# Performance work log

Measured on AMD Instinct MI355X. Metric: run time of the kernel, lower is better.

## Reference

```python
import jax, jax.numpy as jnp
import numpy as np

N_ATOMS = 50000
N_EDGES = 1_600_000
H = 128
EPS = 1e-3  # keras BatchNormalization default epsilon


def _bn(x, gamma, beta, mean, var):
    # inference-mode batch norm with moving statistics
    return gamma * (x - mean) * jax.lax.rsqrt(var + EPS) + beta


def setup_inputs() -> dict:
    key = jax.random.key(0)
    ks = jax.random.split(key, 16)
    s = 0.05
    D1 = H + 1
    inp = {
        "atom_embedding": jax.random.normal(ks[0], (N_ATOMS, H), jnp.float32),
        "bond_embedding": jax.random.normal(ks[1], (N_EDGES, H), jnp.float32),
        "indices_i": jax.random.randint(ks[2], (N_EDGES,), 0, N_ATOMS, dtype=jnp.int32),
        "indices_j": jax.random.randint(ks[3], (N_EDGES,), 0, N_ATOMS, dtype=jnp.int32),
        # preprocess: Dense(3H -> H+1, no bias) + BN, Dense(H+1 -> H+1, no bias) + BN
        "W1": jax.random.normal(ks[4], (3 * H, D1), jnp.float32) * s,
        "g1": jnp.ones((D1,), jnp.float32),
        "b1": jnp.zeros((D1,), jnp.float32),
        "m1": jnp.zeros((D1,), jnp.float32),
        "v1": jnp.ones((D1,), jnp.float32),
        "W2": jax.random.normal(ks[5], (D1, D1), jnp.float32) * s,
        "g2": jnp.ones((D1,), jnp.float32),
        "b2": jnp.zeros((D1,), jnp.float32),
        "m2": jnp.zeros((D1,), jnp.float32),
        "v2": jnp.ones((D1,), jnp.float32),
        # two residual layers, each: x + (x@w1+b1)@w2+b2 (activation=None)
        "r1w1": jax.random.normal(ks[6], (H, H), jnp.float32) * s,
        "r1b1": jnp.zeros((H,), jnp.float32),
        "r1w2": jax.random.normal(ks[7], (H, H), jnp.float32) * s,
        "r1b2": jnp.zeros((H,), jnp.float32),
        "r2w1": jax.random.normal(ks[8], (H, H), jnp.float32) * s,
        "r2b1": jnp.zeros((H,), jnp.float32),
        "r2w2": jax.random.normal(ks[9], (H, H), jnp.float32) * s,
        "r2b2": jnp.zeros((H,), jnp.float32),
    }
    return inp


def reference(atom_embedding, bond_embedding, indices_i, indices_j,
              W1, g1, b1, m1, v1, W2, g2, b2, m2, v2,
              r1w1, r1b1, r1w2, r1b2, r2w1, r2b1, r2w2, r2b2):
    # gather endpoints: [E, H]
    ai = atom_embedding[indices_i]
    aj = atom_embedding[indices_j]
    x = jnp.concatenate([ai, bond_embedding, aj], axis=-1)  # [E, 3H]
    x = _bn(x @ W1, g1, b1, m1, v1)  # [E, H+1]
    x = _bn(x @ W2, g2, b2, m2, v2)  # [E, H+1]
    msg = x[:, :1] * x[:, 1:]  # gate * message -> [E, H]
    atom = atom_embedding + jax.ops.segment_sum(msg, indices_i, num_segments=N_ATOMS)
    # residual MLPs (activation=None -> identity)
    atom = atom + (atom @ r1w1 + r1b1) @ r1w2 + r1b2
    atom = atom + (atom @ r2w1 + r2b1) @ r2w2 + r2b2
    return atom
```

## Files before the change

### kernel.cpp

```cpp
#include <hip/hip_runtime.h>

#define NA 50000
#define NE 1600000
#define HH 128
#define D1 129
#define EPS 1e-3f

typedef __bf16 bf16_t;
typedef bf16_t bf16x8 __attribute__((ext_vector_type(8)));
typedef bf16_t bf16x4 __attribute__((ext_vector_type(4)));
typedef float f32x4 __attribute__((ext_vector_type(4)));

#define OFF_A1   0
#define OFF_C1   129
#define OFF_A2   258
#define OFF_C2   387
#define OFF_WEFF 516
#define OFF_DVEC (OFF_WEFF + 384*129)
#define OFF_Q1   (OFF_DVEC + 129)
#define OFF_Q2   (OFF_Q1 + 128*128)
#define OFF_q1   (OFF_Q2 + 128*128)
#define OFF_q2   (OFF_q1 + 128)
#define OFF_QF   (OFF_q2 + 128)
#define OFF_qf   (OFF_QF + 128*128)
#define OFF_WMT  (((OFF_qf + 128) + 3) & ~3)
#define OFF_WTT  (OFF_WMT + 9216)
#define OFF_WBT  (OFF_WTT + 9216)
#define OFF_QFT  (OFF_WBT + 9216)
#define OFF_PI   (OFF_QFT + 8192)
#define OFF_PJ   (OFF_PI + NA*D1)
#define OFF_ACC  (OFF_PJ + NA*D1)
#define OFF_ACC2 (OFF_ACC + NA*HH)
#define OFF_CNT  (OFF_ACC2 + NA)
#define OFF_CUR  (OFF_CNT + NA)
#define OFF_EDG  (OFF_CUR + NA)
#define OFF_PART (OFF_EDG + NE)
#define SCAN_NB  ((NA + 255) / 256)

__global__ void k_affine(const float* __restrict__ g1, const float* __restrict__ b1,
                         const float* __restrict__ m1, const float* __restrict__ v1,
                         const float* __restrict__ g2, const float* __restrict__ b2,
                         const float* __restrict__ m2, const float* __restrict__ v2,
                         float* __restrict__ ws) {
    for (int idx = threadIdx.x; idx < 2 * D1; idx += blockDim.x) {
        if (idx < D1) {
            float a = g1[idx] * rsqrtf(v1[idx] + EPS);
            ws[OFF_A1 + idx] = a;
            ws[OFF_C1 + idx] = b1[idx] - m1[idx] * a;
        } else {
            int n = idx - D1;
            float a = g2[n] * rsqrtf(v2[n] + EPS);
            ws[OFF_A2 + n] = a;
            ws[OFF_C2 + n] = b2[n] - m2[n] * a;
        }
    }
}

__global__ void k_weff(const float* __restrict__ W1, const float* __restrict__ W2,
                       float* __restrict__ ws) {
    int idx = blockIdx.x * blockDim.x + threadIdx.x;
    if (idx >= 384 * D1 + D1) return;
    const float* a1 = ws + OFF_A1;
    const float* c1 = ws + OFF_C1;
    const float* a2 = ws + OFF_A2;
    const float* c2 = ws + OFF_C2;
    if (idx < 384 * D1) {
        int k = idx / D1, n = idx % D1;
        float s = 0.f;
        for (int t = 0; t < D1; ++t)
            s += W1[(size_t)k * D1 + t] * a1[t] * W2[(size_t)t * D1 + n];
        ws[OFF_WEFF + idx] = s * a2[n];
    } else {
        int n = idx - 384 * D1;
        float s = 0.f;
        for (int t = 0; t < D1; ++t)
            s += c1[t] * W2[(size_t)t * D1 + n];
        ws[OFF_DVEC + n] = s * a2[n] + c2[n];
    }
}

__global__ void k_resid(const float* __restrict__ r1w1, const float* __restrict__ r1b1,
                        const float* __restrict__ r1w2, const float* __restrict__ r1b2,
                        const float* __restrict__ r2w1, const float* __restrict__ r2b1,
                        const float* __restrict__ r2w2, const float* __restrict__ r2b2,
                        float* __restrict__ ws) {
    int idx = blockIdx.x * blockDim.x + threadIdx.x;
    if (idx >= 2 * (128 * 128 + 128)) return;
    int layer = idx / (128 * 128 + 128);
    int r = idx % (128 * 128 + 128);
    const float* w1 = layer ? r2w1 : r1w1;
    const float* b1 = layer ? r2b1 : r1b1;
    const float* w2 = layer ? r2w2 : r1w2;
    const float* b2 = layer ? r2b2 : r1b2;
    float* Q = ws + (layer ? OFF_Q2 : OFF_Q1);
    float* q = ws + (layer ? OFF_q2 : OFF_q1);
    if (r < 128 * 128) {
        int i = r >> 7, j = r & 127;
        float s = (i == j) ? 1.f : 0.f;
        for (int t = 0; t < 128; ++t)
            s += w1[i * 128 + t] * w2[t * 128 + j];
        Q[r] = s;
    } else {
        int j = r - 128 * 128;
        float s = b2[j];
        for (int t = 0; t < 128; ++t)
            s += b1[t] * w2[t * 128 + j];
        q[j] = s;
    }
}

__global__ void k_qf(float* __restrict__ ws) {
    int idx = blockIdx.x * blockDim.x + threadIdx.x;
    if (idx >= 128 * 128 + 128) return;
    const float* Q1 = ws + OFF_Q1;
    const float* Q2 = ws + OFF_Q2;
    if (idx < 128 * 128) {
        int i = idx >> 7, j = idx & 127;
        float s = 0.f;
        for (int m = 0; m < 128; ++m)
            s += Q1[i * 128 + m] * Q2[m * 128 + j];
        ws[OFF_QF + idx] = s;
    } else {
        int j = idx - 128 * 128;
        const float* q1 = ws + OFF_q1;
        float s = ws[OFF_q2 + j];
        for (int m = 0; m < 128; ++m)
            s += q1[m] * Q2[m * 128 + j];
        ws[OFF_qf + j] = s;
    }
}

__global__ void k_pack(float* __restrict__ ws) {
    int idx = blockIdx.x * blockDim.x + threadIdx.x;
    const float* Weff = ws + OFF_WEFF;
    if (idx < 18432) {
        int n = idx >> 7, k = idx & 127;
        float v = (n < 128) ? Weff[(size_t)(128 + k) * D1 + n + 1]
                            : ((n == 128) ? Weff[(size_t)(128 + k) * D1] : 0.f);
        ((bf16_t*)(ws + OFF_WMT))[idx] = (bf16_t)v;
    } else if (idx < 2 * 18432) {
        int r = idx - 18432;
        int n = r >> 7, k = r & 127;
        float v = (n < D1) ? Weff[(size_t)k * D1 + n] : 0.f;
        ((bf16_t*)(ws + OFF_WTT))[r] = (bf16_t)v;
    } else if (idx < 3 * 18432) {
        int r = idx - 2 * 18432;
        int n = r >> 7, k = r & 127;
        float v = (n < D1) ? Weff[(size_t)(256 + k) * D1 + n] : 0.f;
        ((bf16_t*)(ws + OFF_WBT))[r] = (bf16_t)v;
    } else if (idx < 3 * 18432 + 16384) {
        int r = idx - 3 * 18432;
        int n = r >> 7, k = r & 127;
        ((bf16_t*)(ws + OFF_QFT))[r] = (bf16_t)ws[OFF_QF + k * 128 + n];
    }
}

__global__ void k_hist(const int* __restrict__ idx_i, float* __restrict__ ws) {
    int e = blockIdx.x * blockDim.x + threadIdx.x;
    if (e < NE) atomicAdd((int*)(ws + OFF_CNT) + idx_i[e], 1);
}

__global__ void k_scan1(float* __restrict__ ws) {
    const int* cnt = (const int*)(ws + OFF_CNT);
    int i = blockIdx.x * 256 + threadIdx.x;
    int v = (i < NA) ? cnt[i] : 0;
#pragma unroll
    for (int o = 1; o < 64; o <<= 1) v += __shfl_xor(v, o);
    __shared__ int wsum[4];
    if ((threadIdx.x & 63) == 0) wsum[threadIdx.x >> 6] = v;
    __syncthreads();
    if (threadIdx.x == 0)
        ((int*)(ws + OFF_PART))[blockIdx.x] = wsum[0] + wsum[1] + wsum[2] + wsum[3];
}

__global__ void k_scan2(float* __restrict__ ws) {
    int* part = (int*)(ws + OFF_PART);
    __shared__ int ps[256];
    int t = threadIdx.x;
    int v = (t < SCAN_NB) ? part[t] : 0;
    ps[t] = v;
    __syncthreads();
    for (int o = 1; o < 256; o <<= 1) {
        int u = (t >= o) ? ps[t - o] : 0;
        __syncthreads();
        ps[t] += u;
        __syncthreads();
    }
    part[t] = t ? ps[t - 1] : 0;
}

__global__ void k_scan3(float* __restrict__ ws) {
    const int* cnt = (const int*)(ws + OFF_CNT);
    int* cursor = (int*)(ws + OFF_CUR);
    int base = ((const int*)(ws + OFF_PART))[blockIdx.x];
    int i = blockIdx.x * 256 + threadIdx.x;
    int v = (i < NA) ? cnt[i] : 0;
    int lane = threadIdx.x & 63, w = threadIdx.x >> 6;
    int s = v;
#pragma unroll
    for (int o = 1; o < 64; o <<= 1) {
        int u = __shfl_up(s, o);
        if (lane >= o) s += u;
    }
    __shared__ int wtot[4];
    if (lane == 63) wtot[w] = s;
    __syncthreads();
    int add = 0;
    for (int k = 0; k < 4; ++k)
        if (k < w) add += wtot[k];
    if (i < NA) cursor[i] = base + add + s - v;
}

__global__ void k_scatter(const int* __restrict__ idx_i, float* __restrict__ ws) {
    int e = blockIdx.x * blockDim.x + threadIdx.x;
    if (e < NE) {
        int i = idx_i[e];
        int p = atomicAdd((int*)(ws + OFF_CUR) + i, 1);
        ((int*)(ws + OFF_EDG))[p] = e;
    }
}

__global__ __launch_bounds__(256) void k_gemm_mfma(
    const float* __restrict__ A, const float* __restrict__ A2,
    const float* __restrict__ Pi, const float* __restrict__ acc2,
    const bf16_t* __restrict__ Wt, const float* __restrict__ bias,
    float* __restrict__ C, int ldc, int N, int ntiles, int M) {
    __shared__ __align__(16) bf16_t As[64][136];
    int t = threadIdx.x;
    int m0 = blockIdx.x * 64;
#pragma unroll
    for (int it = 0; it < 8; ++it) {
        int idx = t + 256 * it;
        int r = idx >> 5, c4 = idx & 31;
        int grow = m0 + r;
        float4 v = make_float4(0.f, 0.f, 0.f, 0.f);
        if (grow < M) {
            v = ((const float4*)(A + (size_t)grow * 128))[c4];
            if (A2) {
                float4 w = ((const float4*)(A2 + (size_t)grow * 128))[c4];
                v.x += w.x; v.y += w.y; v.z += w.z; v.w += w.w;
            }
            if (acc2) {
                float s = acc2[grow];
                const float* p = Pi + (size_t)grow * D1 + 1 + c4 * 4;
                v.x += s * p[0]; v.y += s * p[1]; v.z += s * p[2]; v.w += s * p[3];
            }
        }
        bf16x4 tmp;
        tmp[0] = (bf16_t)v.x; tmp[1] = (bf16_t)v.y; tmp[2] = (bf16_t)v.z; tmp[3] = (bf16_t)v.w;
        *(bf16x4*)&As[r][c4 * 4] = tmp;
    }
    __syncthreads();
    int lane = t & 63, w = t >> 6;
    int ll = lane & 15, quad = lane >> 4;
    bf16x8 a[4];
#pragma unroll
    for (int k = 0; k < 4; ++k)
        a[k] = *(const bf16x8*)&As[w * 16 + ll][k * 32 + quad * 8];
    for (int nt = 0; nt < ntiles; ++nt) {
        const bf16_t* bp = Wt + (size_t)(nt * 16 + ll) * 128 + quad * 8;
        f32x4 acc = {0.f, 0.f, 0.f, 0.f};
#pragma unroll
        for (int k = 0; k < 4; ++k) {
            bf16x8 b = *(const bf16x8*)(bp + k * 32);
            acc = __builtin_amdgcn_mfma_f32_16x16x32_bf16(a[k], b, acc, 0, 0, 0);
        }
        int col = nt * 16 + ll;
        if (col < N) {
            float bv = bias ? bias[col] : 0.f;
#pragma unroll
            for (int r = 0; r < 4; ++r) {
                int row = m0 + w * 16 + quad * 4 + r;
                if (row < M) C[(size_t)row * ldc + col] = acc[r] + bv;
            }
        }
    }
}

__global__ __launch_bounds__(256) void k_pipj(
    const float* __restrict__ A, const bf16_t* __restrict__ Wt,
    const float* __restrict__ bias, float* __restrict__ Ct,
    const bf16_t* __restrict__ Wb, float* __restrict__ Cb, int M) {
    __shared__ __align__(16) bf16_t As[64][136];
    int t = threadIdx.x;
    int m0 = blockIdx.x * 64;
#pragma unroll
    for (int it = 0; it < 8; ++it) {
        int idx = t + 256 * it;
        int r = idx >> 5, c4 = idx & 31;
        int grow = m0 + r;
        float4 v = make_float4(0.f, 0.f, 0.f, 0.f);
        if (grow < M) v = ((const float4*)(A + (size_t)grow * 128))[c4];
        bf16x4 tmp;
        tmp[0] = (bf16_t)v.x; tmp[1] = (bf16_t)v.y; tmp[2] = (bf16_t)v.z; tmp[3] = (bf16_t)v.w;
        *(bf16x4*)&As[r][c4 * 4] = tmp;
    }
    __syncthreads();
    int lane = t & 63, w = t >> 6;
    int ll = lane & 15, quad = lane >> 4;
    bf16x8 a[4];
#pragma unroll
    for (int k = 0; k < 4; ++k)
        a[k] = *(const bf16x8*)&As[w * 16 + ll][k * 32 + quad * 8];
    for (int half = 0; half < 2; ++half) {
        const bf16_t* W = half ? Wb : Wt;
        float* C = half ? Cb : Ct;
        for (int nt = 0; nt < 9; ++nt) {
            const bf16_t* bp = W + (size_t)(nt * 16 + ll) * 128 + quad * 8;
            f32x4 acc = {0.f, 0.f, 0.f, 0.f};
#pragma unroll
            for (int k = 0; k < 4; ++k) {
                bf16x8 b = *(const bf16x8*)(bp + k * 32);
                acc = __builtin_amdgcn_mfma_f32_16x16x32_bf16(a[k], b, acc, 0, 0, 0);
            }
            int col = nt * 16 + ll;
            if (col < D1) {
                float bv = (half == 0 && bias) ? bias[col] : 0.f;
#pragma unroll
                for (int r = 0; r < 4; ++r) {
                    int row = m0 + w * 16 + quad * 4 + r;
                    if (row < M) C[(size_t)row * D1 + col] = acc[r] + bv;
                }
            }
        }
    }
}

__global__ __launch_bounds__(256) void k_edge_mfma(
    const float* __restrict__ bond, const int* __restrict__ idx_i,
    const int* __restrict__ idx_j, const int* __restrict__ edge_of,
    const bf16_t* __restrict__ WmidT,
    const float* __restrict__ Pi, const float* __restrict__ Pj,
    float* __restrict__ accb, float* __restrict__ acc2) {
    __shared__ __align__(16) bf16_t As[64][136];
    __shared__ int e_s[64], ii_s[64], jj_s[64];

    int t = threadIdx.x;
    size_t p0 = (size_t)blockIdx.x * 64;
    if (t < 64) {
        int e = edge_of[p0 + t];
        e_s[t] = e;
        ii_s[t] = idx_i[e];
        jj_s[t] = idx_j[e];
    }
    __syncthreads();
#pragma unroll
    for (int it = 0; it < 8; ++it) {
        int idx = t + 256 * it;
        int r = idx >> 5, c4 = idx & 31;
        float4 v = ((const float4*)(bond + (size_t)e_s[r] * 128))[c4];
        bf16x4 tmp;
        tmp[0] = (bf16_t)v.x; tmp[1] = (bf16_t)v.y; tmp[2] = (bf16_t)v.z; tmp[3] = (bf16_t)v.w;
        *(bf16x4*)&As[r][c4 * 4] = tmp;
    }
    __syncthreads();
    int lane = t & 63, w = t >> 6;
    int ll = lane & 15, quad = lane >> 4;
    bf16x8 a[4];
#pragma unroll
    for (int k = 0; k < 4; ++k)
        a[k] = *(const bf16x8*)&As[w * 16 + ll][k * 32 + quad * 8];

    int base = w * 16;
    int my = ii_s[base + ll];
    int pv = ll ? ii_s[base + ll - 1] : my;
    unsigned runmask = (unsigned)(__ballot(lane < 16 && my != pv) & 0xFFFFull);

    int jo[4];
#pragma unroll
    for (int r = 0; r < 4; ++r) {
        int e = base + quad * 4 + r;
        jo[r] = jj_s[e] * (D1 * 4) + 4;
    }

    f32x4 ag = {0.f, 0.f, 0.f, 0.f};
    {
        const bf16_t* bp = WmidT + (size_t)(128 + ll) * 128 + quad * 8;
#pragma unroll
        for (int k = 0; k < 4; ++k) {
            bf16x8 b = *(const bf16x8*)(bp + k * 32);
            ag = __builtin_amdgcn_mfma_f32_16x16x32_bf16(a[k], b, ag, 0, 0, 0);
        }
    }
    float g[4];
    int src = lane & 48;
#pragma unroll
    for (int r = 0; r < 4; ++r) {
        float v = ag[r];
        if (ll == 0) {
            int e = base + quad * 4 + r;
            v += Pi[(size_t)ii_s[e] * D1] + Pj[(size_t)jj_s[e] * D1];
        }
        g[r] = __shfl(v, src);
    }

    {
        int rs = 0;
        while (rs < 16) {
            unsigned rest = runmask >> (rs + 1);
            int re = rest ? rs + 1 + __builtin_ctz(rest) : 16;
            float s = 0.f;
#pragma unroll
            for (int r = 0; r < 4; ++r) {
                int e = quad * 4 + r;
                if (e >= rs && e < re) s += g[r];
            }
            s += __shfl_xor(s, 16);
            s += __shfl_xor(s, 32);
            if (lane == 0) atomicAdd(&acc2[ii_s[base + rs]], s);
            rs = re;
        }
    }

    const char* Pjb = (const char*)Pj;
    for (int nt = 0; nt < 8; ++nt) {
        const bf16_t* bp = WmidT + (size_t)(nt * 16 + ll) * 128 + quad * 8;
        f32x4 acc = {0.f, 0.f, 0.f, 0.f};
#pragma unroll
        for (int k = 0; k < 4; ++k) {
            bf16x8 b = *(const bf16x8*)(bp + k * 32);
            acc = __builtin_amdgcn_mfma_f32_16x16x32_bf16(a[k], b, acc, 0, 0, 0);
        }
        int n = nt * 16 + ll;
        float m[4];
#pragma unroll
        for (int r = 0; r < 4; ++r) {
            float y = acc[r] + *(const float*)(Pjb + (size_t)jo[r] + n * 4);
            m[r] = g[r] * y;
        }
        int rs = 0;
        while (rs < 16) {
            unsigned rest = runmask >> (rs + 1);
            int re = rest ? rs + 1 + __builtin_ctz(rest) : 16;
            float s = 0.f;
#pragma unroll
            for (int r = 0; r < 4; ++r) {
                int e = quad * 4 + r;
                if (e >= rs && e < re) s += m[r];
            }
            s += __shfl_xor(s, 16);
            s += __shfl_xor(s, 32);
            if (quad == 0) atomicAdd(&accb[(size_t)ii_s[base + rs] * 128 + n], s);
            rs = re;
        }
    }
}

extern "C" void kernel_launch(void* const* d_in, const int* in_sizes, int n_in,
                              void* d_out, int out_size, void* d_ws, size_t ws_size,
                              hipStream_t stream) {
    const float* atom = (const float*)d_in[0];
    const float* bond = (const float*)d_in[1];
    const int* idx_i = (const int*)d_in[2];
    const int* idx_j = (const int*)d_in[3];
    const float* W1 = (const float*)d_in[4];
    const float* g1 = (const float*)d_in[5];
    const float* b1 = (const float*)d_in[6];
    const float* m1 = (const float*)d_in[7];
    const float* v1 = (const float*)d_in[8];
    const float* W2 = (const float*)d_in[9];
    const float* g2 = (const float*)d_in[10];
    const float* b2 = (const float*)d_in[11];
    const float* m2 = (const float*)d_in[12];
    const float* v2 = (const float*)d_in[13];
    const float* r1w1 = (const float*)d_in[14];
    const float* r1b1 = (const float*)d_in[15];
    const float* r1w2 = (const float*)d_in[16];
    const float* r1b2 = (const float*)d_in[17];
    const float* r2w1 = (const float*)d_in[18];
    const float* r2b1 = (const float*)d_in[19];
    const float* r2w2 = (const float*)d_in[20];
    const float* r2b2 = (const float*)d_in[21];
    float* ws = (float*)d_ws;
    float* out = (float*)d_out;

    hipMemsetAsync(ws + OFF_ACC, 0, (size_t)(NA * HH + 2 * NA) * sizeof(float), stream);

    k_hist<<<(NE + 255) / 256, 256, 0, stream>>>(idx_i, ws);
    k_scan1<<<SCAN_NB, 256, 0, stream>>>(ws);
    k_scan2<<<1, 256, 0, stream>>>(ws);
    k_scan3<<<SCAN_NB, 256, 0, stream>>>(ws);
    k_scatter<<<(NE + 255) / 256, 256, 0, stream>>>(idx_i, ws);

    k_affine<<<1, 256, 0, stream>>>(g1, b1, m1, v1, g2, b2, m2, v2, ws);
    k_weff<<<(384 * D1 + D1 + 255) / 256, 256, 0, stream>>>(W1, W2, ws);
    k_resid<<<(2 * (128 * 128 + 128) + 255) / 256, 256, 0, stream>>>(
        r1w1, r1b1, r1w2, r1b2, r2w1, r2b1, r2w2, r2b2, ws);
    k_qf<<<(128 * 128 + 128 + 255) / 256, 256, 0, stream>>>(ws);
    k_pack<<<(3 * 18432 + 16384 + 255) / 256, 256, 0, stream>>>(ws);

    int gblocks = (NA + 63) / 64;
    k_pipj<<<gblocks, 256, 0, stream>>>(
        atom, (const bf16_t*)(ws + OFF_WTT), ws + OFF_DVEC, ws + OFF_PI,
        (const bf16_t*)(ws + OFF_WBT), ws + OFF_PJ, NA);

    k_edge_mfma<<<NE / 64, 256, 0, stream>>>(
        bond, idx_i, idx_j, (const int*)(ws + OFF_EDG), (const bf16_t*)(ws + OFF_WMT),
        ws + OFF_PI, ws + OFF_PJ, ws + OFF_ACC, ws + OFF_ACC2);

    k_gemm_mfma<<<gblocks, 256, 0, stream>>>(
        atom, ws + OFF_ACC, ws + OFF_PI, ws + OFF_ACC2, (const bf16_t*)(ws + OFF_QFT),
        ws + OFF_qf, out, 128, 128, 8, NA);
}
```

Baseline: 1.831 ms.

## Process four edge tiles per block with LDS-staged weights and prefetch

The edge kernel now handles 256 edges per block in four 64-edge tiles instead of one tile per block. The 144x128 bf16 weight matrix is loaded once into swizzled shared memory rather than read from global memory per MFMA. Bond rows and indices for the next tile are prefetched into registers and written into a second LDS buffer while the current tile computes. It also separates the MFMA/product phase from the atomic scatter phase. The cost is much more LDS per block (about 72 KB) and more registers, which lowers occupancy.

```diff
diff --git a/kernel.cpp b/kernel.cpp
--- a/kernel.cpp
+++ b/kernel.cpp
@@ -332,117 +332,178 @@
     const bf16_t* __restrict__ WmidT,
     const float* __restrict__ Pi, const float* __restrict__ Pj,
     float* __restrict__ accb, float* __restrict__ acc2) {
-    __shared__ __align__(16) bf16_t As[64][136];
-    __shared__ int e_s[64], ii_s[64], jj_s[64];
+    __shared__ __align__(16) bf16_t Bs[144 * 128];
+    __shared__ __align__(16) bf16_t As[2][64][136];
+    __shared__ int e_all[256];
+    __shared__ int ii2[2][64], jj2[2][64];
 
     int t = threadIdx.x;
-    size_t p0 = (size_t)blockIdx.x * 64;
-    if (t < 64) {
-        int e = edge_of[p0 + t];
-        e_s[t] = e;
-        ii_s[t] = idx_i[e];
-        jj_s[t] = idx_j[e];
-    }
-    __syncthreads();
+    size_t p0 = (size_t)blockIdx.x * 256;
+    e_all[t] = edge_of[p0 + t];
+
+    {
+        const float4* src = (const float4*)WmidT;
+#pragma unroll
+        for (int k = 0; k < 9; ++k) {
+            int idx16 = t + 256 * k;
+            int g = idx16 << 4;
+            int row = g >> 8;
+            int swz = (g & 255) ^ ((row & 7) << 4);
+            *(float4*)((char*)Bs + row * 256 + swz) = src[idx16];
+        }
+    }
+    __syncthreads();
+
 #pragma unroll
     for (int it = 0; it < 8; ++it) {
         int idx = t + 256 * it;
         int r = idx >> 5, c4 = idx & 31;
-        float4 v = ((const float4*)(bond + (size_t)e_s[r] * 128))[c4];
+        float4 v = ((const float4*)(bond + (size_t)e_all[r] * 128))[c4];
         bf16x4 tmp;
         tmp[0] = (bf16_t)v.x; tmp[1] = (bf16_t)v.y; tmp[2] = (bf16_t)v.z; tmp[3] = (bf16_t)v.w;
-        *(bf16x4*)&As[r][c4 * 4] = tmp;
-    }
-    __syncthreads();
+        *(bf16x4*)&As[0][r][c4 * 4] = tmp;
+    }
+    if (t < 64) {
+        int e = e_all[t];
+        ii2[0][t] = idx_i[e];
+        jj2[0][t] = idx_j[e];
+    }
+    __syncthreads();
+
     int lane = t & 63, w = t >> 6;
     int ll = lane & 15, quad = lane >> 4;
-    bf16x8 a[4];
-#pragma unroll
-    for (int k = 0; k < 4; ++k)
-        a[k] = *(const bf16x8*)&As[w * 16 + ll][k * 32 + quad * 8];
-
     int base = w * 16;
-    int my = ii_s[base + ll];
-    int pv = ll ? ii_s[base + ll - 1] : my;
-    unsigned runmask = (unsigned)(__ballot(lane < 16 && my != pv) & 0xFFFFull);
-
-    int jo[4];
-#pragma unroll
-    for (int r = 0; r < 4; ++r) {
-        int e = base + quad * 4 + r;
-        jo[r] = jj_s[e] * (D1 * 4) + 4;
-    }
-
-    f32x4 ag = {0.f, 0.f, 0.f, 0.f};
-    {
-        const bf16_t* bp = WmidT + (size_t)(128 + ll) * 128 + quad * 8;
+    int src_lane = lane & 48;
+
+    for (int tt = 0; tt < 4; ++tt) {
+        int buf = tt & 1;
+        bf16x8 a[4];
+#pragma unroll
+        for (int k = 0; k < 4; ++k)
+            a[k] = *(const bf16x8*)&As[buf][base + ll][k * 32 + quad * 8];
+
+        int my = ii2[buf][base + ll];
+        int pv = ll ? ii2[buf][base + ll - 1] : my;
+        unsigned runmask = (unsigned)(__ballot(lane < 16 && my != pv) & 0xFFFFull);
+        int jo[4];
+#pragma unroll
+        for (int r = 0; r < 4; ++r)
+            jo[r] = jj2[buf][base + quad * 4 + r] * (D1 * 4) + 4;
+        float gp[4] = {0.f, 0.f, 0.f, 0.f};
+        if (ll == 0) {
+#pragma unroll
+            for (int r = 0; r < 4; ++r) {
+                int e = base + quad * 4 + r;
+                gp[r] = Pi[(size_t)ii2[buf][e] * D1] + Pj[(size_t)jj2[buf][e] * D1];
+            }
+        }
+
+        float4 pf[8];
+        int ni = 0, nj = 0;
+        if (tt < 3) {
+            int nb = (tt + 1) * 64;
+#pragma unroll
+            for (int it = 0; it < 8; ++it) {
+                int idx = t + 256 * it;
+                int r = idx >> 5, c4 = idx & 31;
+                pf[it] = ((const float4*)(bond + (size_t)e_all[nb + r] * 128))[c4];
+            }
+            if (t < 64) {
+                int e = e_all[nb + t];
+                ni = idx_i[e];
+                nj = idx_j[e];
+            }
+        }
+
+        f32x4 ag = {0.f, 0.f, 0.f, 0.f};
 #pragma unroll
         for (int k = 0; k < 4; ++k) {
-            bf16x8 b = *(const bf16x8*)(bp + k * 32);
+            int row = 128 + ll;
+            int colb = (quad * 16 + k * 64) ^ ((row & 7) << 4);
+            bf16x8 b = *(const bf16x8*)((const char*)Bs + row * 256 + colb);
             ag = __builtin_amdgcn_mfma_f32_16x16x32_bf16(a[k], b, ag, 0, 0, 0);
         }
-    }
-    float g[4];
-    int src = lane & 48;
-#pragma unroll
-    for (int r = 0; r < 4; ++r) {
-        float v = ag[r];
-        if (ll == 0) {
-            int e = base + quad * 4 + r;
-            v += Pi[(size_t)ii_s[e] * D1] + Pj[(size_t)jj_s[e] * D1];
-        }
-        g[r] = __shfl(v, src);
-    }
-
-    {
-        int rs = 0;
-        while (rs < 16) {
-            unsigned rest = runmask >> (rs + 1);
-            int re = rest ? rs + 1 + __builtin_ctz(rest) : 16;
-            float s = 0.f;
-#pragma unroll
-            for (int r = 0; r < 4; ++r) {
-                int e = quad * 4 + r;
-                if (e >= rs && e < re) s += g[r];
-            }
-            s += __shfl_xor(s, 16);
-            s += __shfl_xor(s, 32);
-            if (lane == 0) atomicAdd(&acc2[ii_s[base + rs]], s);
-            rs = re;
-        }
-    }
-
-    const char* Pjb = (const char*)Pj;
-    for (int nt = 0; nt < 8; ++nt) {
-        const bf16_t* bp = WmidT + (size_t)(nt * 16 + ll) * 128 + quad * 8;
-        f32x4 acc = {0.f, 0.f, 0.f, 0.f};
-#pragma unroll
-        for (int k = 0; k < 4; ++k) {
-            bf16x8 b = *(const bf16x8*)(bp + k * 32);
-            acc = __builtin_amdgcn_mfma_f32_16x16x32_bf16(a[k], b, acc, 0, 0, 0);
-        }
-        int n = nt * 16 + ll;
-        float m[4];
+        float g[4];
 #pragma unroll
         for (int r = 0; r < 4; ++r) {
-            float y = acc[r] + *(const float*)(Pjb + (size_t)jo[r] + n * 4);
-            m[r] = g[r] * y;
-        }
-        int rs = 0;
-        while (rs < 16) {
-            unsigned rest = runmask >> (rs + 1);
-            int re = rest ? rs + 1 + __builtin_ctz(rest) : 16;
-            float s = 0.f;
-#pragma unroll
-            for (int r = 0; r < 4; ++r) {
-                int e = quad * 4 + r;
-                if (e >= rs && e < re) s += m[r];
-            }
-            s += __shfl_xor(s, 16);
-            s += __shfl_xor(s, 32);
-            if (quad == 0) atomicAdd(&accb[(size_t)ii_s[base + rs] * 128 + n], s);
-            rs = re;
-        }
+            float v = ag[r];
+            if (ll == 0) v += gp[r];
+            g[r] = __shfl(v, src_lane);
+        }
+
+        f32x4 mm[8];
+#pragma unroll
+        for (int nt = 0; nt < 8; ++nt) {
+            float pjv[4];
+#pragma unroll
+            for (int r = 0; r < 4; ++r)
+                pjv[r] = *(const float*)((const char*)Pj + (size_t)jo[r] + (nt * 16 + ll) * 4);
+            f32x4 acc = {0.f, 0.f, 0.f, 0.f};
+#pragma unroll
+            for (int k = 0; k < 4; ++k) {
+                int row = nt * 16 + ll;
+                int colb = (quad * 16 + k * 64) ^ ((row & 7) << 4);
+                bf16x8 b = *(const bf16x8*)((const char*)Bs + row * 256 + colb);
+                acc = __builtin_amdgcn_mfma_f32_16x16x32_bf16(a[k], b, acc, 0, 0, 0);
+            }
+#pragma unroll
+            for (int r = 0; r < 4; ++r) mm[nt][r] = g[r] * (acc[r] + pjv[r]);
+        }
+
+        if (tt < 3) {
+            int nbuf = buf ^ 1;
+#pragma unroll
+            for (int it = 0; it < 8; ++it) {
+                int idx = t + 256 * it;
+                int r = idx >> 5, c4 = idx & 31;
+                bf16x4 tmp;
+                tmp[0] = (bf16_t)pf[it].x; tmp[1] = (bf16_t)pf[it].y;
+                tmp[2] = (bf16_t)pf[it].z; tmp[3] = (bf16_t)pf[it].w;
+                *(bf16x4*)&As[nbuf][r][c4 * 4] = tmp;
+            }
+            if (t < 64) {
+                ii2[nbuf][t] = ni;
+                jj2[nbuf][t] = nj;
+            }
+        }
+
+        {
+            int rs = 0;
+            while (rs < 16) {
+                unsigned rest = runmask >> (rs + 1);
+                int re = rest ? rs + 1 + __builtin_ctz(rest) : 16;
+                float s = 0.f;
+#pragma unroll
+                for (int r = 0; r < 4; ++r) {
+                    int e = quad * 4 + r;
+                    if (e >= rs && e < re) s += g[r];
+                }
+                s += __shfl_xor(s, 16);
+                s += __shfl_xor(s, 32);
+                if (lane == 0) atomicAdd(&acc2[ii2[buf][base + rs]], s);
+                rs = re;
+            }
+        }
+#pragma unroll
+        for (int nt = 0; nt < 8; ++nt) {
+            int n = nt * 16 + ll;
+            int rs = 0;
+            while (rs < 16) {
+                unsigned rest = runmask >> (rs + 1);
+                int re = rest ? rs + 1 + __builtin_ctz(rest) : 16;
+                float s = 0.f;
+#pragma unroll
+                for (int r = 0; r < 4; ++r) {
+                    int e = quad * 4 + r;
+                    if (e >= rs && e < re) s += mm[nt][r];
+                }
+                s += __shfl_xor(s, 16);
+                s += __shfl_xor(s, 32);
+                if (quad == 0) atomicAdd(&accb[(size_t)ii2[buf][base + rs] * 128 + n], s);
+                rs = re;
+            }
+        }
+        __syncthreads();
     }
 }
 
@@ -494,7 +555,7 @@
         atom, (const bf16_t*)(ws + OFF_WTT), ws + OFF_DVEC, ws + OFF_PI,
         (const bf16_t*)(ws + OFF_WBT), ws + OFF_PJ, NA);
 
-    k_edge_mfma<<<NE / 64, 256, 0, stream>>>(
+    k_edge_mfma<<<NE / 256, 256, 0, stream>>>(
         bond, idx_i, idx_j, (const int*)(ws + OFF_EDG), (const bf16_t*)(ws + OFF_WMT),
         ws + OFF_PI, ws + OFF_PJ, ws + OFF_ACC, ws + OFF_ACC2);
 
```

Result: faster. 1.645 ms (-10.1%).

## Restructure edge kernel: waves split output columns, weights held in registers, no LDS

Applied to the files above, without the earlier changes.

Before, each wave owned 16 edges and walked all 128 output columns, reloading weight fragments from global memory. Now each wave owns two 16-column output tiles plus the gate column and keeps those weight fragments in registers for the whole block. Each block loops over 256 sorted edges in groups of 16, loading bond rows straight into MFMA A fragments and dropping the LDS staging and barriers. The catch is that every wave now gathers every bond row, so global bond reads become redundant across the four waves, and the grid shrinks fourfold.

```diff
diff --git a/kernel.cpp b/kernel.cpp
--- a/kernel.cpp
+++ b/kernel.cpp
@@ -332,116 +332,127 @@
     const bf16_t* __restrict__ WmidT,
     const float* __restrict__ Pi, const float* __restrict__ Pj,
     float* __restrict__ accb, float* __restrict__ acc2) {
-    __shared__ __align__(16) bf16_t As[64][136];
-    __shared__ int e_s[64], ii_s[64], jj_s[64];
-
     int t = threadIdx.x;
-    size_t p0 = (size_t)blockIdx.x * 64;
-    if (t < 64) {
-        int e = edge_of[p0 + t];
-        e_s[t] = e;
-        ii_s[t] = idx_i[e];
-        jj_s[t] = idx_j[e];
-    }
-    __syncthreads();
-#pragma unroll
-    for (int it = 0; it < 8; ++it) {
-        int idx = t + 256 * it;
-        int r = idx >> 5, c4 = idx & 31;
-        float4 v = ((const float4*)(bond + (size_t)e_s[r] * 128))[c4];
-        bf16x4 tmp;
-        tmp[0] = (bf16_t)v.x; tmp[1] = (bf16_t)v.y; tmp[2] = (bf16_t)v.z; tmp[3] = (bf16_t)v.w;
-        *(bf16x4*)&As[r][c4 * 4] = tmp;
-    }
-    __syncthreads();
     int lane = t & 63, w = t >> 6;
     int ll = lane & 15, quad = lane >> 4;
-    bf16x8 a[4];
-#pragma unroll
-    for (int k = 0; k < 4; ++k)
-        a[k] = *(const bf16x8*)&As[w * 16 + ll][k * 32 + quad * 8];
-
-    int base = w * 16;
-    int my = ii_s[base + ll];
-    int pv = ll ? ii_s[base + ll - 1] : my;
-    unsigned runmask = (unsigned)(__ballot(lane < 16 && my != pv) & 0xFFFFull);
-
-    int jo[4];
-#pragma unroll
-    for (int r = 0; r < 4; ++r) {
-        int e = base + quad * 4 + r;
-        jo[r] = jj_s[e] * (D1 * 4) + 4;
-    }
-
-    f32x4 ag = {0.f, 0.f, 0.f, 0.f};
+    size_t p0 = (size_t)blockIdx.x * 256;
+
+    bf16x8 bg[4], bn0[4], bn1[4];
     {
-        const bf16_t* bp = WmidT + (size_t)(128 + ll) * 128 + quad * 8;
+        const bf16_t* gp = WmidT + (size_t)(128 + ll) * 128 + quad * 8;
+        const bf16_t* q0 = WmidT + (size_t)((w * 2) * 16 + ll) * 128 + quad * 8;
+        const bf16_t* q1 = WmidT + (size_t)((w * 2 + 1) * 16 + ll) * 128 + quad * 8;
 #pragma unroll
         for (int k = 0; k < 4; ++k) {
-            bf16x8 b = *(const bf16x8*)(bp + k * 32);
-            ag = __builtin_amdgcn_mfma_f32_16x16x32_bf16(a[k], b, ag, 0, 0, 0);
-        }
-    }
-    float g[4];
-    int src = lane & 48;
-#pragma unroll
-    for (int r = 0; r < 4; ++r) {
-        float v = ag[r];
-        if (ll == 0) {
-            int e = base + quad * 4 + r;
-            v += Pi[(size_t)ii_s[e] * D1] + Pj[(size_t)jj_s[e] * D1];
-        }
-        g[r] = __shfl(v, src);
-    }
-
-    {
-        int rs = 0;
-        while (rs < 16) {
-            unsigned rest = runmask >> (rs + 1);
-            int re = rest ? rs + 1 + __builtin_ctz(rest) : 16;
-            float s = 0.f;
-#pragma unroll
-            for (int r = 0; r < 4; ++r) {
-                int e = quad * 4 + r;
-                if (e >= rs && e < re) s += g[r];
-            }
-            s += __shfl_xor(s, 16);
-            s += __shfl_xor(s, 32);
-            if (lane == 0) atomicAdd(&acc2[ii_s[base + rs]], s);
-            rs = re;
-        }
-    }
-
-    const char* Pjb = (const char*)Pj;
-    for (int nt = 0; nt < 8; ++nt) {
-        const bf16_t* bp = WmidT + (size_t)(nt * 16 + ll) * 128 + quad * 8;
-        f32x4 acc = {0.f, 0.f, 0.f, 0.f};
+            bg[k] = *(const bf16x8*)(gp + k * 32);
+            bn0[k] = *(const bf16x8*)(q0 + k * 32);
+            bn1[k] = *(const bf16x8*)(q1 + k * 32);
+        }
+    }
+    int n0 = (w * 2) * 16 + ll, n1 = (w * 2 + 1) * 16 + ll;
+
+    for (int g = 0; g < 16; ++g) {
+        int base = g * 16;
+        int e = edge_of[p0 + base + ll];
+        int iv = idx_i[e], jv = idx_j[e];
+        int ipv = __shfl(iv, (ll + 15) & 15);
+        unsigned bmask = (unsigned)(__ballot(ll > 0 && iv != ipv) & 0xFFFFu);
+        int jr[4], ir[4];
+#pragma unroll
+        for (int r = 0; r < 4; ++r) {
+            jr[r] = __shfl(jv, quad * 4 + r);
+            ir[r] = __shfl(iv, quad * 4 + r);
+        }
+
+        const float4* brow = (const float4*)(bond + (size_t)e * 128);
+        bf16x8 a[4];
 #pragma unroll
         for (int k = 0; k < 4; ++k) {
-            bf16x8 b = *(const bf16x8*)(bp + k * 32);
-            acc = __builtin_amdgcn_mfma_f32_16x16x32_bf16(a[k], b, acc, 0, 0, 0);
-        }
-        int n = nt * 16 + ll;
-        float m[4];
+            float4 u = brow[k * 8 + quad * 2];
+            float4 v = brow[k * 8 + quad * 2 + 1];
+            bf16x8 tmp;
+            tmp[0] = (bf16_t)u.x; tmp[1] = (bf16_t)u.y;
+            tmp[2] = (bf16_t)u.z; tmp[3] = (bf16_t)u.w;
+            tmp[4] = (bf16_t)v.x; tmp[5] = (bf16_t)v.y;
+            tmp[6] = (bf16_t)v.z; tmp[7] = (bf16_t)v.w;
+            a[k] = tmp;
+        }
+
+        f32x4 ag = {0.f, 0.f, 0.f, 0.f};
+#pragma unroll
+        for (int k = 0; k < 4; ++k)
+            ag = __builtin_amdgcn_mfma_f32_16x16x32_bf16(a[k], bg[k], ag, 0, 0, 0);
+        float gl[4];
 #pragma unroll
         for (int r = 0; r < 4; ++r) {
-            float y = acc[r] + *(const float*)(Pjb + (size_t)jo[r] + n * 4);
-            m[r] = g[r] * y;
-        }
-        int rs = 0;
-        while (rs < 16) {
-            unsigned rest = runmask >> (rs + 1);
-            int re = rest ? rs + 1 + __builtin_ctz(rest) : 16;
-            float s = 0.f;
-#pragma unroll
-            for (int r = 0; r < 4; ++r) {
-                int e = quad * 4 + r;
-                if (e >= rs && e < re) s += m[r];
-            }
-            s += __shfl_xor(s, 16);
-            s += __shfl_xor(s, 32);
-            if (quad == 0) atomicAdd(&accb[(size_t)ii_s[base + rs] * 128 + n], s);
-            rs = re;
+            float v = ag[r];
+            if (ll == 0) v += Pi[(size_t)ir[r] * D1] + Pj[(size_t)jr[r] * D1];
+            gl[r] = __shfl(v, lane & 48);
+        }
+
+        if (w == 0) {
+            int rs = 0;
+            while (rs < 16) {
+                unsigned rest = bmask >> (rs + 1);
+                int re = rest ? rs + 1 + __builtin_ctz(rest) : 16;
+                float s = 0.f;
+#pragma unroll
+                for (int r = 0; r < 4; ++r) {
+                    int ee = quad * 4 + r;
+                    if (ee >= rs && ee < re) s += gl[r];
+                }
+                s += __shfl_xor(s, 16);
+                s += __shfl_xor(s, 32);
+                int irs = __shfl(iv, rs);
+                if (lane == 0) atomicAdd(&acc2[irs], s);
+                rs = re;
+            }
+        }
+
+        float pj0[4], pj1[4];
+#pragma unroll
+        for (int r = 0; r < 4; ++r) {
+            const float* pjr = Pj + (size_t)jr[r] * D1 + 1;
+            pj0[r] = pjr[n0];
+            pj1[r] = pjr[n1];
+        }
+        f32x4 ac0 = {0.f, 0.f, 0.f, 0.f}, ac1 = {0.f, 0.f, 0.f, 0.f};
+#pragma unroll
+        for (int k = 0; k < 4; ++k)
+            ac0 = __builtin_amdgcn_mfma_f32_16x16x32_bf16(a[k], bn0[k], ac0, 0, 0, 0);
+#pragma unroll
+        for (int k = 0; k < 4; ++k)
+            ac1 = __builtin_amdgcn_mfma_f32_16x16x32_bf16(a[k], bn1[k], ac1, 0, 0, 0);
+        float m0[4], m1[4];
+#pragma unroll
+        for (int r = 0; r < 4; ++r) {
+            m0[r] = gl[r] * (ac0[r] + pj0[r]);
+            m1[r] = gl[r] * (ac1[r] + pj1[r]);
+        }
+
+        {
+            int rs = 0;
+            while (rs < 16) {
+                unsigned rest = bmask >> (rs + 1);
+                int re = rest ? rs + 1 + __builtin_ctz(rest) : 16;
+                float s0 = 0.f, s1 = 0.f;
+#pragma unroll
+                for (int r = 0; r < 4; ++r) {
+                    int ee = quad * 4 + r;
+                    if (ee >= rs && ee < re) { s0 += m0[r]; s1 += m1[r]; }
+                }
+                s0 += __shfl_xor(s0, 16);
+                s0 += __shfl_xor(s0, 32);
+                s1 += __shfl_xor(s1, 16);
+                s1 += __shfl_xor(s1, 32);
+                int irs = __shfl(iv, rs);
+                if (quad == 0) {
+                    float* ab = accb + (size_t)irs * 128;
+                    atomicAdd(ab + n0, s0);
+                    atomicAdd(ab + n1, s1);
+                }
+                rs = re;
+            }
         }
     }
 }
@@ -494,7 +505,7 @@
         atom, (const bf16_t*)(ws + OFF_WTT), ws + OFF_DVEC, ws + OFF_PI,
         (const bf16_t*)(ws + OFF_WBT), ws + OFF_PJ, NA);
 
-    k_edge_mfma<<<NE / 64, 256, 0, stream>>>(
+    k_edge_mfma<<<NE / 256, 256, 0, stream>>>(
         bond, idx_i, idx_j, (const int*)(ws + OFF_EDG), (const bf16_t*)(ws + OFF_WMT),
         ws + OFF_PI, ws + OFF_PJ, ws + OFF_ACC, ws + OFF_ACC2);
 
```

Result: slower. 1.915 ms (+4.6%).
